# Optimization experiments

Hardware: AMD Instinct MI355X
Metric: run time of the kernel (lower is better)

Reference implementation:

```python
import jax, jax.numpy as jnp
import numpy as np

BS, S, DIM, H = 4, 2048, 1024, 16
DH = DIM // H  # 64


def setup_inputs() -> dict:
    key = jax.random.key(0)
    ks = jax.random.split(key, 12)
    def lin(k, fan_in):
        bound = 1.0 / np.sqrt(fan_in)
        kw, kb = jax.random.split(k)
        W = jax.random.uniform(kw, (DIM, DIM), jnp.float32, -bound, bound)
        b = jax.random.uniform(kb, (DIM,), jnp.float32, -bound, bound)
        return W, b
    Wq, bq = lin(ks[0], DIM)
    Wk, bk = lin(ks[1], DIM)
    Wv, bv = lin(ks[2], DIM)
    Wo, bo = lin(ks[3], DIM)
    return {
        "query": jax.random.normal(ks[4], (BS, S, DIM), jnp.float32),
        "key": jax.random.normal(ks[5], (BS, S, DIM), jnp.float32),
        "value": jax.random.normal(ks[6], (BS, S, DIM), jnp.float32),
        "mask": jnp.ones((BS, S), jnp.int32),
        "Wq": Wq, "bq": bq, "Wk": Wk, "bk": bk,
        "Wv": Wv, "bv": bv, "Wo": Wo, "bo": bo,
    }


def reference(query, key, value, mask, Wq, bq, Wk, bk, Wv, bv, Wo, bo):
    bs, q_len, dim = query.shape
    def shape_heads(x):  # (bs, s, dim) -> (bs, H, s, DH)
        return x.reshape(bs, -1, H, DH).transpose(0, 2, 1, 3)
    # Linear projections (torch Linear: x @ W.T + b)
    q = shape_heads(query @ Wq.T + bq)
    k = shape_heads(key @ Wk.T + bk)
    v = shape_heads(value @ Wv.T + bv)
    q = q / jnp.sqrt(jnp.asarray(DH, q.dtype))
    # scores: (bs, H, q_len, k_len)
    scores = jnp.einsum('bhqd,bhkd->bhqk', q, k)
    neg = jnp.asarray(-jnp.inf, scores.dtype)
    pad = (mask == 0)[:, None, None, :]  # (bs,1,1,k_len)
    scores = jnp.where(pad, neg, scores)
    weights = jax.nn.softmax(scores, axis=-1)
    # dropout is identity in eval mode (reference is deterministic)
    context = jnp.einsum('bhqk,bhkd->bhqd', weights, v)
    context = context.transpose(0, 2, 1, 3).reshape(bs, q_len, dim)
    return context @ Wo.T + bo
```

## Files before the change

kernel.cpp:

```cpp
#include <hip/hip_runtime.h>
#include <hip/hip_bf16.h>
#include <math.h>

#define BSZ 4
#define SEQ 2048
#define DIMN 1024
#define NHEAD 16
#define DHEAD 64
#define MROWS (BSZ*SEQ)

typedef __bf16 bf16x8 __attribute__((ext_vector_type(8)));
typedef float  f32x4  __attribute__((ext_vector_type(4)));
typedef float  f32x16 __attribute__((ext_vector_type(16)));
typedef float  fvec4  __attribute__((ext_vector_type(4)));
typedef short  s16x4  __attribute__((ext_vector_type(4)));
typedef short  s16x8  __attribute__((ext_vector_type(8)));

__device__ __forceinline__ short f2bf(float v) {
  __hip_bfloat16 b = __float2bfloat16(v);
  return *reinterpret_cast<short*>(&b);
}
__device__ __forceinline__ float bf2f(short s) {
  __hip_bfloat16 b = *reinterpret_cast<__hip_bfloat16*>(&s);
  return __bfloat162float(b);
}

__device__ __forceinline__ void gld_lds16(const void* g, void* l) {
  __builtin_amdgcn_global_load_lds((const __attribute__((address_space(1))) void*)g,
                                   (__attribute__((address_space(3))) void*)l, 16, 0, 0);
}

#define QSC 0.18033688011112042f

__global__ __launch_bounds__(256) void pack_w4(
    const float* __restrict__ Wq, const float* __restrict__ Wk,
    const float* __restrict__ Wv, const float* __restrict__ Wo,
    short* __restrict__ WQh, short* __restrict__ WKh,
    short* __restrict__ WVh, short* __restrict__ WOh, short* __restrict__ WOl,
    long n)
{
  long i = ((long)blockIdx.x * 256 + threadIdx.x) * 4;
  if (i >= n) return;
  int which = blockIdx.y;
  if (which == 3) {
    fvec4 v = *(const fvec4*)&Wo[i];
    s16x4 h, l;
#pragma unroll
    for (int j = 0; j < 4; ++j) {
      short hb = f2bf(v[j]);
      h[j] = hb;
      l[j] = f2bf(v[j] - bf2f(hb));
    }
    *(s16x4*)&WOh[i] = h;
    *(s16x4*)&WOl[i] = l;
  } else {
    const float* src = which == 0 ? Wq : (which == 1 ? Wk : Wv);
    short* dst = which == 0 ? WQh : (which == 1 ? WKh : WVh);
    float sc = which == 0 ? QSC : 1.f;
    fvec4 v = *(const fvec4*)&src[i];
    s16x4 h;
#pragma unroll
    for (int j = 0; j < 4; ++j) h[j] = f2bf(v[j] * sc);
    *(s16x4*)&dst[i] = h;
  }
}

__global__ __launch_bounds__(256) void pack_hi3(
    const float* __restrict__ q, const float* __restrict__ k,
    const float* __restrict__ v,
    short* __restrict__ xq, short* __restrict__ xk, short* __restrict__ xv,
    long n)
{
  long i = ((long)blockIdx.x * 256 + threadIdx.x) * 4;
  if (i >= n) return;
  const float* src = blockIdx.y == 0 ? q : (blockIdx.y == 1 ? k : v);
  short* dst = blockIdx.y == 0 ? xq : (blockIdx.y == 1 ? xk : xv);
  fvec4 x = *(const fvec4*)&src[i];
  s16x4 h;
#pragma unroll
  for (int j = 0; j < 4; ++j) h[j] = f2bf(x[j]);
  *(s16x4*)&dst[i] = h;
}

__global__ __launch_bounds__(256) void maskbias_k(
    const int* __restrict__ mask, float* __restrict__ mb, int n)
{
  int i = blockIdx.x * 256 + threadIdx.x;
  if (i < n) mb[i] = mask[i] ? 0.f : -1e30f;
}

__global__ __launch_bounds__(64) void mask_flags(
    const int* __restrict__ mask, int* __restrict__ flg)
{
  int c = blockIdx.x;
  int base = (c >> 4) * SEQ + (c & 15) * 128;
  int m0 = mask[base + threadIdx.x];
  int m1 = mask[base + 64 + threadIdx.x];
  unsigned long long bal = __ballot(m0 != 0 && m1 != 0);
  if (threadIdx.x == 0) flg[c] = (bal == ~0ull) ? 1 : 0;
}

__global__ __launch_bounds__(256) void gemm_h(
    const short* __restrict__ A, const short* __restrict__ B,
    const float* __restrict__ bias, float bscale,
    float* __restrict__ Cf, short* __restrict__ Cb,
    int M, int N, int K, int mode)
{
  __shared__ __align__(16) short sA[128*32];
  __shared__ __align__(16) short sB[128*32];
  const int t = threadIdx.x;
  const int ln = t & 15, quad = (t & 63) >> 4, w = t >> 6;
  const int wm = w >> 1, wn = w & 1;
  const int m0 = blockIdx.y * 128, n0 = blockIdx.x * 128;
  const int lrow = t >> 2;
  const int lko = (((t & 3) ^ ((t >> 3) & 3))) * 8;
  const int fsw = ((ln >> 1) & 3);
  f32x4 acc[4][4];
#pragma unroll
  for (int i = 0; i < 4; ++i)
#pragma unroll
    for (int j = 0; j < 4; ++j) acc[i][j] = (f32x4){0.f,0.f,0.f,0.f};

  for (int k0 = 0; k0 < K; k0 += 32) {
    __syncthreads();
#pragma unroll
    for (int u = 0; u < 2; ++u) {
      int row = u*64 + lrow;
      gld_lds16(A + (size_t)(m0+row)*K + k0 + lko, sA + u*2048 + t*8);
      gld_lds16(B + (size_t)(n0+row)*K + k0 + lko, sB + u*2048 + t*8);
    }
    __syncthreads();
    bf16x8 af[4], bfr[4];
#pragma unroll
    for (int mt = 0; mt < 4; ++mt)
      af[mt] = *(bf16x8*)&sA[(wm*64 + mt*16 + ln)*32 + (quad ^ fsw)*8];
#pragma unroll
    for (int nt = 0; nt < 4; ++nt)
      bfr[nt] = *(bf16x8*)&sB[(wn*64 + nt*16 + ln)*32 + (quad ^ fsw)*8];
#pragma unroll
    for (int mt = 0; mt < 4; ++mt)
#pragma unroll
      for (int nt = 0; nt < 4; ++nt)
        acc[mt][nt] = __builtin_amdgcn_mfma_f32_16x16x32_bf16(af[mt], bfr[nt], acc[mt][nt], 0, 0, 0);
  }
#pragma unroll
  for (int nt = 0; nt < 4; ++nt) {
    int col = n0 + wn*64 + nt*16 + ln;
    float bv = bias[col] * bscale;
    if (mode == 2) {
      int hd = col >> 6, dd = col & 63;
#pragma unroll
      for (int mt = 0; mt < 4; ++mt) {
        int sg = m0 + wm*64 + mt*16 + quad*4;
        int b = sg >> 11, s = sg & 2047;
        s16x4 h;
#pragma unroll
        for (int r = 0; r < 4; ++r) h[r] = f2bf(acc[mt][nt][r] + bv);
        *(s16x4*)&Cb[((size_t)((b*16 + hd)*64 + dd))*SEQ + s] = h;
      }
    } else {
#pragma unroll
      for (int mt = 0; mt < 4; ++mt)
#pragma unroll
        for (int r = 0; r < 4; ++r) {
          int row = m0 + wm*64 + mt*16 + quad*4 + r;
          float val = acc[mt][nt][r] + bv;
          if (mode == 0) Cf[(size_t)row*N + col] = val;
          else           Cb[(size_t)row*N + col] = f2bf(val);
        }
    }
  }
}

__global__ __launch_bounds__(256) void gemm_sp(
    const short* __restrict__ Ah, const short* __restrict__ Al,
    const short* __restrict__ Bh, const short* __restrict__ Bl,
    const float* __restrict__ bias, float bscale,
    float* __restrict__ C, int M, int N, int K)
{
  __shared__ __align__(16) short sA[2*128*32];
  __shared__ __align__(16) short sB[2*128*32];
  const int t = threadIdx.x;
  const int ln = t & 15, quad = (t & 63) >> 4, w = t >> 6;
  const int wm = w >> 1, wn = w & 1;
  const int m0 = blockIdx.y * 128, n0 = blockIdx.x * 128;
  const int lrow = t >> 2;
  const int lko = (((t & 3) ^ ((t >> 3) & 3))) * 8;
  const int fsw = ((ln >> 1) & 3);
  f32x4 acc[4][4];
#pragma unroll
  for (int i = 0; i < 4; ++i)
#pragma unroll
    for (int j = 0; j < 4; ++j) acc[i][j] = (f32x4){0.f,0.f,0.f,0.f};

  for (int k0 = 0; k0 < K; k0 += 32) {
    __syncthreads();
#pragma unroll
    for (int u = 0; u < 2; ++u) {
      int row = u*64 + lrow;
      gld_lds16(Ah + (size_t)(m0+row)*K + k0 + lko, sA + u*2048 + t*8);
      gld_lds16(Al + (size_t)(m0+row)*K + k0 + lko, sA + 4096 + u*2048 + t*8);
      gld_lds16(Bh + (size_t)(n0+row)*K + k0 + lko, sB + u*2048 + t*8);
      gld_lds16(Bl + (size_t)(n0+row)*K + k0 + lko, sB + 4096 + u*2048 + t*8);
    }
    __syncthreads();
    bf16x8 ah[4], al[4], bh[4], bl[4];
#pragma unroll
    for (int mt = 0; mt < 4; ++mt) {
      int r = wm*64 + mt*16 + ln;
      ah[mt] = *(bf16x8*)&sA[r*32 + (quad ^ fsw)*8];
      al[mt] = *(bf16x8*)&sA[4096 + r*32 + (quad ^ fsw)*8];
    }
#pragma unroll
    for (int nt = 0; nt < 4; ++nt) {
      int r = wn*64 + nt*16 + ln;
      bh[nt] = *(bf16x8*)&sB[r*32 + (quad ^ fsw)*8];
      bl[nt] = *(bf16x8*)&sB[4096 + r*32 + (quad ^ fsw)*8];
    }
#pragma unroll
    for (int mt = 0; mt < 4; ++mt)
#pragma unroll
      for (int nt = 0; nt < 4; ++nt) {
        acc[mt][nt] = __builtin_amdgcn_mfma_f32_16x16x32_bf16(ah[mt], bh[nt], acc[mt][nt], 0, 0, 0);
        acc[mt][nt] = __builtin_amdgcn_mfma_f32_16x16x32_bf16(ah[mt], bl[nt], acc[mt][nt], 0, 0, 0);
        acc[mt][nt] = __builtin_amdgcn_mfma_f32_16x16x32_bf16(al[mt], bh[nt], acc[mt][nt], 0, 0, 0);
      }
  }
#pragma unroll
  for (int nt = 0; nt < 4; ++nt) {
    float bv = bias[n0 + wn*64 + nt*16 + ln] * bscale;
#pragma unroll
    for (int mt = 0; mt < 4; ++mt)
#pragma unroll
      for (int r = 0; r < 4; ++r)
        C[(size_t)(m0 + wm*64 + mt*16 + quad*4 + r)*N + (n0 + wn*64 + nt*16 + ln)] =
            acc[mt][nt][r] + bv;
  }
}

__global__ __launch_bounds__(256, 3) void attn_32(
    const short* __restrict__ QB, const short* __restrict__ KB,
    const short* __restrict__ VT, const float* __restrict__ mb,
    const int* __restrict__ flg,
    short* __restrict__ CTXh, short* __restrict__ CTXl)
{
  __shared__ __align__(16) short lds[16384];
  short* sK = lds;
  short* sV = lds + 8192;

  const int t = threadIdx.x;
  const int l31 = t & 31, hi = (t >> 5) & 1, w = t >> 6;
  const int gb = blockIdx.x;
  const int chunk = gb >> 3, qt128 = chunk & 15, bh = ((chunk >> 4) << 3) + (gb & 7);
  const int b = bh >> 4, hd = bh & 15;

#pragma unroll
  for (int i = 0; i < 4; ++i) {
    int u = i*256 + t;
    int row = u >> 3, gr = (u & 7) ^ (row & 7);
    gld_lds16(QB + ((size_t)(b*SEQ + qt128*128 + row))*DIMN + hd*64 + gr*8,
              sK + u*8);
  }
  __syncthreads();
  const int q = w*32 + l31;
  bf16x8 qf[4];
#pragma unroll
  for (int ks = 0; ks < 4; ++ks)
    qf[ks] = *(bf16x8*)&sK[q*64 + ((ks*2 + hi) ^ (q & 7))*8];

  f32x16 o_acc[2] = {};
  float m_run = -1e30f, l_run = 0.f;

  for (int kt = 0; kt < SEQ/128; ++kt) {
    __syncthreads();
#pragma unroll
    for (int i = 0; i < 4; ++i) {
      int u = i*256 + t;
      { int row = u >> 3, gr = (u & 7) ^ (row & 7);
        gld_lds16(KB + ((size_t)(b*SEQ + kt*128 + row))*DIMN + hd*64 + gr*8,
                  sK + u*8); }
      { int d = u >> 4, gr = (u & 15) ^ (d & 15);
        gld_lds16(VT + ((size_t)(bh*64 + d))*SEQ + kt*128 + gr*8,
                  sV + u*8); }
    }
    __syncthreads();

    f32x16 sacc[4] = {};
#pragma unroll
    for (int ks = 0; ks < 4; ++ks)
#pragma unroll
      for (int mt = 0; mt < 4; ++mt) {
        int kc = mt*32 + l31;
        bf16x8 kf = *(bf16x8*)&sK[kc*64 + ((ks*2 + hi) ^ (kc & 7))*8];
        sacc[mt] = __builtin_amdgcn_mfma_f32_32x32x16_bf16(kf, qf[ks], sacc[mt], 0, 0, 0);
      }

    if (!flg[b*16 + kt]) {
#pragma unroll
      for (int mt = 0; mt < 4; ++mt)
#pragma unroll
        for (int r = 0; r < 16; ++r)
          sacc[mt][r] += mb[b*SEQ + kt*128 + mt*32 + (r&3) + 8*(r>>2) + 4*hi];
    }

    float tmax = -1e30f;
#pragma unroll
    for (int mt = 0; mt < 4; ++mt)
#pragma unroll
      for (int r = 0; r < 16; ++r) tmax = fmaxf(tmax, sacc[mt][r]);
    tmax = fmaxf(tmax, __shfl_xor(tmax, 32));

    if (!__all(tmax <= m_run + 8.f)) {
      float mnew = fmaxf(m_run, tmax);
      float alpha = exp2f(m_run - mnew);
      l_run *= alpha;
#pragma unroll
      for (int dt = 0; dt < 2; ++dt)
#pragma unroll
        for (int r = 0; r < 16; ++r) o_acc[dt][r] *= alpha;
      m_run = mnew;
    }

    float rs = 0.f;
#pragma unroll
    for (int mt = 0; mt < 4; ++mt)
#pragma unroll
      for (int r = 0; r < 16; ++r) {
        float p = exp2f(sacc[mt][r] - m_run);
        sacc[mt][r] = p;
        rs += p;
      }
    rs += __shfl_xor(rs, 32);
    l_run += rs;

#pragma unroll
    for (int mt = 0; mt < 4; ++mt) {
      unsigned wv[8];
#pragma unroll
      for (int i = 0; i < 8; ++i) {
        float plo = sacc[mt][2*i], phi = sacc[mt][2*i+1];
        asm("v_cvt_pk_bf16_f32 %0, %1, %2" : "=v"(wv[i]) : "v"(plo), "v"(phi));
      }
#pragma unroll
      for (int h = 0; h < 2; ++h) {
        unsigned f0 = wv[h*4+0], f1 = wv[h*4+1], f2 = wv[h*4+2], f3 = wv[h*4+3];
        asm volatile("v_permlane32_swap_b32 %0, %1" : "+v"(f0), "+v"(f2));
        asm volatile("v_permlane32_swap_b32 %0, %1" : "+v"(f1), "+v"(f3));
        union { unsigned u[4]; bf16x8 v; } pu;
        pu.u[0] = f0; pu.u[1] = f1; pu.u[2] = f2; pu.u[3] = f3;
        const int kcs = mt*2 + h;
#pragma unroll
        for (int dt = 0; dt < 2; ++dt) {
          int d = dt*32 + l31;
          bf16x8 vf = *(bf16x8*)&sV[d*128 + ((kcs*2 + hi) ^ (d & 15))*8];
          o_acc[dt] = __builtin_amdgcn_mfma_f32_32x32x16_bf16(vf, pu.v, o_acc[dt], 0, 0, 0);
        }
      }
    }
  }

  float invl = (l_run > 0.f) ? 1.f / l_run : 0.f;
  const size_t rowbase = (size_t)(b*SEQ + qt128*128 + q)*DIMN + hd*64;
#pragma unroll
  for (int dt = 0; dt < 2; ++dt)
#pragma unroll
    for (int rg = 0; rg < 4; ++rg) {
      s16x4 hq, lq;
#pragma unroll
      for (int r2 = 0; r2 < 4; ++r2) {
        float val = o_acc[dt][rg*4 + r2] * invl;
        short hb = f2bf(val);
        hq[r2] = hb;
        lq[r2] = f2bf(val - bf2f(hb));
      }
      size_t idx = rowbase + dt*32 + rg*8 + hi*4;
      *(s16x4*)&CTXh[idx] = hq;
      *(s16x4*)&CTXl[idx] = lq;
    }
}

__global__ __launch_bounds__(256) void gemm_bt(
    const float* __restrict__ X, const float* __restrict__ W,
    const float* __restrict__ bias, float* __restrict__ C,
    int M, int N, int K)
{
  __shared__ __align__(16) float Xs[16][68];
  __shared__ __align__(16) float Ws[16][68];
  const int t  = threadIdx.x;
  const int tx = t & 15, ty = t >> 4;
  const int m0 = blockIdx.y << 6, n0 = blockIdx.x << 6;
  const int ldr = t >> 2;
  const int lk  = (t & 3) << 2;
  float acc[4][4] = {{0.f}};
  const float* Xp = X + (size_t)(m0 + ldr) * K + lk;
  const float* Wp = W + (size_t)(n0 + ldr) * K + lk;
  for (int k0 = 0; k0 < K; k0 += 16) {
    float4 xa = *(const float4*)(Xp + k0);
    float4 wa = *(const float4*)(Wp + k0);
    Xs[lk+0][ldr]=xa.x; Xs[lk+1][ldr]=xa.y; Xs[lk+2][ldr]=xa.z; Xs[lk+3][ldr]=xa.w;
    Ws[lk+0][ldr]=wa.x; Ws[lk+1][ldr]=wa.y; Ws[lk+2][ldr]=wa.z; Ws[lk+3][ldr]=wa.w;
    __syncthreads();
#pragma unroll
    for (int kk = 0; kk < 16; ++kk) {
      float4 a4 = *(const float4*)&Xs[kk][ty<<2];
      float4 b4 = *(const float4*)&Ws[kk][tx<<2];
      float av[4] = {a4.x, a4.y, a4.z, a4.w};
      float bv[4] = {b4.x, b4.y, b4.z, b4.w};
#pragma unroll
      for (int i = 0; i < 4; ++i)
#pragma unroll
        for (int j = 0; j < 4; ++j)
          acc[i][j] = fmaf(av[i], bv[j], acc[i][j]);
    }
    __syncthreads();
  }
  float4 bb4 = *(const float4*)&bias[n0 + (tx<<2)];
  const float bv[4] = {bb4.x, bb4.y, bb4.z, bb4.w};
#pragma unroll
  for (int i = 0; i < 4; ++i) {
    float4 o;
    o.x = acc[i][0]+bv[0]; o.y = acc[i][1]+bv[1];
    o.z = acc[i][2]+bv[2]; o.w = acc[i][3]+bv[3];
    *(float4*)&C[(size_t)(m0 + (ty<<2) + i) * N + n0 + (tx<<2)] = o;
  }
}

__global__ __launch_bounds__(256) void attn_fwd(
    const float* __restrict__ Q, const float* __restrict__ Kbuf,
    const float* __restrict__ Vbuf, const int* __restrict__ mask,
    float* __restrict__ CTX)
{
  __shared__ __align__(16) float Qs[64][68];
  __shared__ __align__(16) float KPs[64][68];
  __shared__ __align__(16) float Vs[64][68];
  const int t  = threadIdx.x;
  const int tx = t & 15, ty = t >> 4;
  const int qt = blockIdx.x;
  const int bh = blockIdx.y;
  const int b  = bh >> 4, h = bh & 15;
  const int ldr = t >> 2;
  const int lcb = (t & 3) << 2;
  const float* Qp = Q + (size_t)(b*SEQ + (qt<<6)) * DIMN + h*DHEAD;
#pragma unroll
  for (int u = 0; u < 4; ++u) {
    int kb = lcb + (u<<4);
    float4 q4 = *(const float4*)(Qp + (size_t)ldr*DIMN + kb);
    Qs[kb+0][ldr]=q4.x; Qs[kb+1][ldr]=q4.y; Qs[kb+2][ldr]=q4.z; Qs[kb+3][ldr]=q4.w;
  }
  float mrow[4], lsum[4], o[4][4];
#pragma unroll
  for (int i = 0; i < 4; ++i) {
    mrow[i] = -1e30f; lsum[i] = 0.f;
#pragma unroll
    for (int j = 0; j < 4; ++j) o[i][j] = 0.f;
  }
  const int qrow0 = ty << 2;
  const int col0  = tx << 2;
  for (int kt = 0; kt < SEQ/64; ++kt) {
    __syncthreads();
    const float* Kp = Kbuf + (size_t)(b*SEQ + (kt<<6)) * DIMN + h*DHEAD;
    const float* Vp = Vbuf + (size_t)(b*SEQ + (kt<<6)) * DIMN + h*DHEAD;
#pragma unroll
    for (int u = 0; u < 4; ++u) {
      int kb = lcb + (u<<4);
      float4 k4 = *(const float4*)(Kp + (size_t)ldr*DIMN + kb);
      KPs[kb+0][ldr]=k4.x; KPs[kb+1][ldr]=k4.y; KPs[kb+2][ldr]=k4.z; KPs[kb+3][ldr]=k4.w;
      float4 v4 = *(const float4*)(Vp + (size_t)ldr*DIMN + kb);
      *(float4*)&Vs[ldr][kb] = v4;
    }
    __syncthreads();
    float s[4][4] = {{0.f}};
#pragma unroll 8
    for (int kk = 0; kk < 64; ++kk) {
      float4 a4 = *(const float4*)&Qs[kk][qrow0];
      float4 b4 = *(const float4*)&KPs[kk][col0];
      float av[4] = {a4.x, a4.y, a4.z, a4.w};
      float bv[4] = {b4.x, b4.y, b4.z, b4.w};
#pragma unroll
      for (int i = 0; i < 4; ++i)
#pragma unroll
        for (int j = 0; j < 4; ++j)
          s[i][j] = fmaf(av[i], bv[j], s[i][j]);
    }
    int mk[4];
#pragma unroll
    for (int j = 0; j < 4; ++j) mk[j] = mask[b*SEQ + (kt<<6) + col0 + j];
    float p[4][4];
#pragma unroll
    for (int i = 0; i < 4; ++i) {
#pragma unroll
      for (int j = 0; j < 4; ++j)
        s[i][j] = mk[j] ? s[i][j]*0.125f : -1e30f;
      float tm = fmaxf(fmaxf(s[i][0], s[i][1]), fmaxf(s[i][2], s[i][3]));
#pragma unroll
      for (int off = 8; off >= 1; off >>= 1)
        tm = fmaxf(tm, __shfl_xor(tm, off, 64));
      float mnew  = fmaxf(mrow[i], tm);
      float aa = __expf(mrow[i] - mnew);
      mrow[i] = mnew;
      float rsum = 0.f;
#pragma unroll
      for (int j = 0; j < 4; ++j) {
        float pv = __expf(s[i][j] - mnew);
        p[i][j] = pv; rsum += pv;
      }
#pragma unroll
      for (int off = 8; off >= 1; off >>= 1)
        rsum += __shfl_xor(rsum, off, 64);
      lsum[i] = lsum[i]*aa + rsum;
#pragma unroll
      for (int j = 0; j < 4; ++j) o[i][j] *= aa;
    }
    __syncthreads();
#pragma unroll
    for (int i = 0; i < 4; ++i)
#pragma unroll
      for (int j = 0; j < 4; ++j)
        KPs[col0 + j][qrow0 + i] = p[i][j];
    __syncthreads();
#pragma unroll 8
    for (int kk = 0; kk < 64; ++kk) {
      float4 a4 = *(const float4*)&KPs[kk][qrow0];
      float4 v4 = *(const float4*)&Vs[kk][col0];
      float av[4] = {a4.x, a4.y, a4.z, a4.w};
      float vv[4] = {v4.x, v4.y, v4.z, v4.w};
#pragma unroll
      for (int i = 0; i < 4; ++i)
#pragma unroll
        for (int j = 0; j < 4; ++j)
          o[i][j] = fmaf(av[i], vv[j], o[i][j]);
    }
  }
  float* Cp = CTX + (size_t)(b*SEQ + (qt<<6)) * DIMN + h*DHEAD;
#pragma unroll
  for (int i = 0; i < 4; ++i) {
    float inv = lsum[i] > 0.f ? 1.0f/lsum[i] : 0.f;
    float4 ov;
    ov.x = o[i][0]*inv; ov.y = o[i][1]*inv;
    ov.z = o[i][2]*inv; ov.w = o[i][3]*inv;
    *(float4*)(Cp + (size_t)(qrow0 + i)*DIMN + col0) = ov;
  }
}

extern "C" void kernel_launch(void* const* d_in, const int* in_sizes, int n_in,
                              void* d_out, int out_size, void* d_ws, size_t ws_size,
                              hipStream_t stream)
{
  const float* query = (const float*)d_in[0];
  const float* key   = (const float*)d_in[1];
  const float* value = (const float*)d_in[2];
  const int*   mask  = (const int*)d_in[3];
  const float* Wq = (const float*)d_in[4];
  const float* bq = (const float*)d_in[5];
  const float* Wk = (const float*)d_in[6];
  const float* bk = (const float*)d_in[7];
  const float* Wv = (const float*)d_in[8];
  const float* bv = (const float*)d_in[9];
  const float* Wo = (const float*)d_in[10];
  const float* bo = (const float*)d_in[11];
  float* out = (float*)d_out;

  const size_t E  = (size_t)MROWS * DIMN;
  const size_t WE = (size_t)DIMN * DIMN;

  const size_t o_XB   = 5*WE*2;
  const size_t o_QB   = o_XB   + 3*E*2;
  const size_t o_KB   = o_QB   + E*2;
  const size_t o_VT   = o_KB   + E*2;
  const size_t o_CTXh = o_VT   + E*2;
  const size_t o_CTXl = o_CTXh + E*2;
  const size_t o_MB   = o_CTXl + E*2;
  const size_t o_FLG  = o_MB   + MROWS*4;
  const size_t NEED   = o_FLG  + 64*4;

  if (ws_size < NEED) {
    const size_t n = E;
    float* Qb = (float*)d_ws;
    float* Kb = Qb + n;
    float* Vb = Kb + n;
    float* Cb = Vb + n;
    dim3 gg(DIMN/64, MROWS/64), blk(256);
    hipLaunchKernelGGL(gemm_bt, gg, blk, 0, stream, query, Wq, bq, Qb, MROWS, DIMN, DIMN);
    hipLaunchKernelGGL(gemm_bt, gg, blk, 0, stream, key,   Wk, bk, Kb, MROWS, DIMN, DIMN);
    hipLaunchKernelGGL(gemm_bt, gg, blk, 0, stream, value, Wv, bv, Vb, MROWS, DIMN, DIMN);
    dim3 ga(SEQ/64, BSZ*NHEAD);
    hipLaunchKernelGGL(attn_fwd, ga, blk, 0, stream, Qb, Kb, Vb, mask, Cb);
    hipLaunchKernelGGL(gemm_bt, gg, blk, 0, stream, Cb, Wo, bo, out, MROWS, DIMN, DIMN);
    return;
  }

  char* Wp = (char*)d_ws;
  short* WQh = (short*)Wp;
  short* WKh = WQh + WE;
  short* WVh = WQh + 2*WE;
  short* WOh = WQh + 3*WE;
  short* WOl = WQh + 4*WE;
  short* XBq  = (short*)(Wp + o_XB);
  short* XBk  = XBq + E;
  short* XBv  = XBk + E;
  short* QB   = (short*)(Wp + o_QB);
  short* KB   = (short*)(Wp + o_KB);
  short* VT   = (short*)(Wp + o_VT);
  short* CTXh = (short*)(Wp + o_CTXh);
  short* CTXl = (short*)(Wp + o_CTXl);
  float* MB   = (float*)(Wp + o_MB);
  int*   FLG  = (int*)(Wp + o_FLG);

  dim3 blk(256);
  dim3 gW(WE/1024, 4), gX(E/1024, 3);
  dim3 gg(DIMN/128, MROWS/128);
  dim3 gat(BSZ*NHEAD*SEQ/128);

  hipLaunchKernelGGL(pack_w4, gW, blk, 0, stream, Wq, Wk, Wv, Wo,
                     WQh, WKh, WVh, WOh, WOl, (long)WE);
  hipLaunchKernelGGL(maskbias_k, dim3(MROWS/256), blk, 0, stream, mask, MB, MROWS);
  hipLaunchKernelGGL(mask_flags, dim3(64), dim3(64), 0, stream, mask, FLG);
  hipLaunchKernelGGL(pack_hi3, gX, blk, 0, stream, query, key, value,
                     XBq, XBk, XBv, (long)E);

  hipLaunchKernelGGL(gemm_h, gg, blk, 0, stream, XBq, WQh, bq, QSC,
                     (float*)nullptr, QB, MROWS, DIMN, DIMN, 1);
  hipLaunchKernelGGL(gemm_h, gg, blk, 0, stream, XBk, WKh, bk, 1.f,
                     (float*)nullptr, KB, MROWS, DIMN, DIMN, 1);
  hipLaunchKernelGGL(gemm_h, gg, blk, 0, stream, XBv, WVh, bv, 1.f,
                     (float*)nullptr, VT, MROWS, DIMN, DIMN, 2);

  hipLaunchKernelGGL(attn_32, gat, blk, 0, stream, QB, KB, VT, MB, FLG, CTXh, CTXl);

  hipLaunchKernelGGL(gemm_sp, gg, blk, 0, stream, CTXh, CTXl, WOh, WOl, bo, 1.f,
                     out, MROWS, DIMN, DIMN);
}
```

Measured before the change: 433.5 us.

## Double-buffer K/V tiles in attention kernel to overlap loads with MFMA

The attention kernel now keeps two LDS buffers for K and V and prefetches the next key tile while computing on the current one, with a single barrier per iteration instead of two. Q is staged in a separate LDS region, and s_setprio raises wave priority around the MFMA sections. The row max is computed with a tree reduction instead of a serial chain. The LDS footprint doubles to 64KB and occupancy hint drops from 3 to 2 blocks per CU, which trades latency hiding across waves for overlap within a block.

```diff
diff --git a/kernel.cpp b/kernel.cpp
--- a/kernel.cpp
+++ b/kernel.cpp
@@ -28,6 +28,17 @@
 __device__ __forceinline__ void gld_lds16(const void* g, void* l) {
   __builtin_amdgcn_global_load_lds((const __attribute__((address_space(1))) void*)g,
                                    (__attribute__((address_space(3))) void*)l, 16, 0, 0);
+}
+
+__device__ __forceinline__ float max16(const f32x16 v) {
+  float m0 = fmaxf(fmaxf(v[0], v[1]),  v[2]);
+  float m1 = fmaxf(fmaxf(v[3], v[4]),  v[5]);
+  float m2 = fmaxf(fmaxf(v[6], v[7]),  v[8]);
+  float m3 = fmaxf(fmaxf(v[9], v[10]), v[11]);
+  float m4 = fmaxf(fmaxf(v[12], v[13]), v[14]);
+  float m5 = fmaxf(v[15], m0);
+  float m6 = fmaxf(fmaxf(m1, m2), m3);
+  return fmaxf(fmaxf(m4, m5), m6);
 }
 
 #define QSC 0.18033688011112042f
@@ -238,15 +249,13 @@
   }
 }
 
-__global__ __launch_bounds__(256, 3) void attn_32(
+__global__ __launch_bounds__(256, 2) void attn_db(
     const short* __restrict__ QB, const short* __restrict__ KB,
     const short* __restrict__ VT, const float* __restrict__ mb,
     const int* __restrict__ flg,
     short* __restrict__ CTXh, short* __restrict__ CTXl)
 {
-  __shared__ __align__(16) short lds[16384];
-  short* sK = lds;
-  short* sV = lds + 8192;
+  __shared__ __align__(16) short lds[32768];
 
   const int t = threadIdx.x;
   const int l31 = t & 31, hi = (t >> 5) & 1, w = t >> 6;
@@ -259,41 +268,60 @@
     int u = i*256 + t;
     int row = u >> 3, gr = (u & 7) ^ (row & 7);
     gld_lds16(QB + ((size_t)(b*SEQ + qt128*128 + row))*DIMN + hd*64 + gr*8,
-              sK + u*8);
+              lds + 16384 + u*8);
+  }
+#pragma unroll
+  for (int i = 0; i < 4; ++i) {
+    int u = i*256 + t;
+    { int row = u >> 3, gr = (u & 7) ^ (row & 7);
+      gld_lds16(KB + ((size_t)(b*SEQ + row))*DIMN + hd*64 + gr*8,
+                lds + u*8); }
+    { int d = u >> 4, gr = (u & 15) ^ (d & 15);
+      gld_lds16(VT + ((size_t)(bh*64 + d))*SEQ + gr*8,
+                lds + 8192 + u*8); }
   }
   __syncthreads();
   const int q = w*32 + l31;
   bf16x8 qf[4];
 #pragma unroll
   for (int ks = 0; ks < 4; ++ks)
-    qf[ks] = *(bf16x8*)&sK[q*64 + ((ks*2 + hi) ^ (q & 7))*8];
+    qf[ks] = *(const bf16x8*)&lds[16384 + q*64 + ((ks*2 + hi) ^ (q & 7))*8];
+  asm volatile("s_waitcnt lgkmcnt(0)" ::: "memory");
+  __builtin_amdgcn_s_barrier();
 
   f32x16 o_acc[2] = {};
   float m_run = -1e30f, l_run = 0.f;
+  int cur = 0;
 
   for (int kt = 0; kt < SEQ/128; ++kt) {
-    __syncthreads();
-#pragma unroll
-    for (int i = 0; i < 4; ++i) {
-      int u = i*256 + t;
-      { int row = u >> 3, gr = (u & 7) ^ (row & 7);
-        gld_lds16(KB + ((size_t)(b*SEQ + kt*128 + row))*DIMN + hd*64 + gr*8,
-                  sK + u*8); }
-      { int d = u >> 4, gr = (u & 15) ^ (d & 15);
-        gld_lds16(VT + ((size_t)(bh*64 + d))*SEQ + kt*128 + gr*8,
-                  sV + u*8); }
-    }
-    __syncthreads();
+    if (kt + 1 < SEQ/128) {
+      short* dK = lds + (cur ^ 1)*16384;
+      short* dV = dK + 8192;
+#pragma unroll
+      for (int i = 0; i < 4; ++i) {
+        int u = i*256 + t;
+        { int row = u >> 3, gr = (u & 7) ^ (row & 7);
+          gld_lds16(KB + ((size_t)(b*SEQ + (kt+1)*128 + row))*DIMN + hd*64 + gr*8,
+                    dK + u*8); }
+        { int d = u >> 4, gr = (u & 15) ^ (d & 15);
+          gld_lds16(VT + ((size_t)(bh*64 + d))*SEQ + (kt+1)*128 + gr*8,
+                    dV + u*8); }
+      }
+    }
+    const short* sK = lds + cur*16384;
+    const short* sV = sK + 8192;
 
     f32x16 sacc[4] = {};
+    __builtin_amdgcn_s_setprio(1);
 #pragma unroll
     for (int ks = 0; ks < 4; ++ks)
 #pragma unroll
       for (int mt = 0; mt < 4; ++mt) {
         int kc = mt*32 + l31;
-        bf16x8 kf = *(bf16x8*)&sK[kc*64 + ((ks*2 + hi) ^ (kc & 7))*8];
+        bf16x8 kf = *(const bf16x8*)&sK[kc*64 + ((ks*2 + hi) ^ (kc & 7))*8];
         sacc[mt] = __builtin_amdgcn_mfma_f32_32x32x16_bf16(kf, qf[ks], sacc[mt], 0, 0, 0);
       }
+    __builtin_amdgcn_s_setprio(0);
 
     if (!flg[b*16 + kt]) {
 #pragma unroll
@@ -303,11 +331,8 @@
           sacc[mt][r] += mb[b*SEQ + kt*128 + mt*32 + (r&3) + 8*(r>>2) + 4*hi];
     }
 
-    float tmax = -1e30f;
-#pragma unroll
-    for (int mt = 0; mt < 4; ++mt)
-#pragma unroll
-      for (int r = 0; r < 16; ++r) tmax = fmaxf(tmax, sacc[mt][r]);
+    float tmax = fmaxf(fmaxf(max16(sacc[0]), max16(sacc[1])),
+                       fmaxf(max16(sacc[2]), max16(sacc[3])));
     tmax = fmaxf(tmax, __shfl_xor(tmax, 32));
 
     if (!__all(tmax <= m_run + 8.f)) {
@@ -333,6 +358,7 @@
     rs += __shfl_xor(rs, 32);
     l_run += rs;
 
+    __builtin_amdgcn_s_setprio(1);
 #pragma unroll
     for (int mt = 0; mt < 4; ++mt) {
       unsigned wv[8];
@@ -352,11 +378,16 @@
 #pragma unroll
         for (int dt = 0; dt < 2; ++dt) {
           int d = dt*32 + l31;
-          bf16x8 vf = *(bf16x8*)&sV[d*128 + ((kcs*2 + hi) ^ (d & 15))*8];
+          bf16x8 vf = *(const bf16x8*)&sV[d*128 + ((kcs*2 + hi) ^ (d & 15))*8];
           o_acc[dt] = __builtin_amdgcn_mfma_f32_32x32x16_bf16(vf, pu.v, o_acc[dt], 0, 0, 0);
         }
       }
     }
+    __builtin_amdgcn_s_setprio(0);
+
+    asm volatile("s_waitcnt vmcnt(0)" ::: "memory");
+    __builtin_amdgcn_s_barrier();
+    cur ^= 1;
   }
 
   float invl = (l_run > 0.f) ? 1.f / l_run : 0.f;
@@ -625,7 +656,7 @@
   hipLaunchKernelGGL(gemm_h, gg, blk, 0, stream, XBv, WVh, bv, 1.f,
                      (float*)nullptr, VT, MROWS, DIMN, DIMN, 2);
 
-  hipLaunchKernelGGL(attn_32, gat, blk, 0, stream, QB, KB, VT, MB, FLG, CTXh, CTXl);
+  hipLaunchKernelGGL(attn_db, gat, blk, 0, stream, QB, KB, VT, MB, FLG, CTXh, CTXl);
 
   hipLaunchKernelGGL(gemm_sp, gg, blk, 0, stream, CTXh, CTXl, WOh, WOl, bo, 1.f,
                      out, MROWS, DIMN, DIMN);
```

New measurement: 441.8 us. About the same (+1.9%).

## Split attention key tile into halves with max folded into MFMA init and setprio

Applied to the files above, without the earlier changes.

The attention inner loop now handles each 128-key tile as two 64-key halves. Score accumulators start at -m_run, so the running-max subtraction rides on the MFMA accumulate, and the online-softmax update runs per half. s_setprio is raised around the MFMA sections and the max reduction is rebalanced into a tree. The goal is lower register pressure from the halved score buffer and shorter dependency chains in the softmax, at the cost of more frequent rescale checks and extra shuffles per tile.

```diff
diff --git a/kernel.cpp b/kernel.cpp
--- a/kernel.cpp
+++ b/kernel.cpp
@@ -28,6 +28,17 @@
 __device__ __forceinline__ void gld_lds16(const void* g, void* l) {
   __builtin_amdgcn_global_load_lds((const __attribute__((address_space(1))) void*)g,
                                    (__attribute__((address_space(3))) void*)l, 16, 0, 0);
+}
+
+__device__ __forceinline__ float max16(const f32x16 v) {
+  float m0 = fmaxf(fmaxf(v[0], v[1]),  v[2]);
+  float m1 = fmaxf(fmaxf(v[3], v[4]),  v[5]);
+  float m2 = fmaxf(fmaxf(v[6], v[7]),  v[8]);
+  float m3 = fmaxf(fmaxf(v[9], v[10]), v[11]);
+  float m4 = fmaxf(fmaxf(v[12], v[13]), v[14]);
+  float m5 = fmaxf(v[15], m0);
+  float m6 = fmaxf(fmaxf(m1, m2), m3);
+  return fmaxf(fmaxf(m4, m5), m6);
 }
 
 #define QSC 0.18033688011112042f
@@ -238,7 +249,7 @@
   }
 }
 
-__global__ __launch_bounds__(256, 3) void attn_32(
+__global__ __launch_bounds__(256, 3) void attn_hp(
     const short* __restrict__ QB, const short* __restrict__ KB,
     const short* __restrict__ VT, const float* __restrict__ mb,
     const int* __restrict__ flg,
@@ -266,10 +277,10 @@
   bf16x8 qf[4];
 #pragma unroll
   for (int ks = 0; ks < 4; ++ks)
-    qf[ks] = *(bf16x8*)&sK[q*64 + ((ks*2 + hi) ^ (q & 7))*8];
+    qf[ks] = *(const bf16x8*)&sK[q*64 + ((ks*2 + hi) ^ (q & 7))*8];
 
   f32x16 o_acc[2] = {};
-  float m_run = -1e30f, l_run = 0.f;
+  float m_run = 0.f, l_run = 0.f;
 
   for (int kt = 0; kt < SEQ/128; ++kt) {
     __syncthreads();
@@ -285,77 +296,103 @@
     }
     __syncthreads();
 
-    f32x16 sacc[4] = {};
-#pragma unroll
-    for (int ks = 0; ks < 4; ++ks)
-#pragma unroll
-      for (int mt = 0; mt < 4; ++mt) {
-        int kc = mt*32 + l31;
-        bf16x8 kf = *(bf16x8*)&sK[kc*64 + ((ks*2 + hi) ^ (kc & 7))*8];
-        sacc[mt] = __builtin_amdgcn_mfma_f32_32x32x16_bf16(kf, qf[ks], sacc[mt], 0, 0, 0);
-      }
-
-    if (!flg[b*16 + kt]) {
-#pragma unroll
-      for (int mt = 0; mt < 4; ++mt)
-#pragma unroll
-        for (int r = 0; r < 16; ++r)
-          sacc[mt][r] += mb[b*SEQ + kt*128 + mt*32 + (r&3) + 8*(r>>2) + 4*hi];
-    }
-
-    float tmax = -1e30f;
-#pragma unroll
-    for (int mt = 0; mt < 4; ++mt)
-#pragma unroll
-      for (int r = 0; r < 16; ++r) tmax = fmaxf(tmax, sacc[mt][r]);
-    tmax = fmaxf(tmax, __shfl_xor(tmax, 32));
-
-    if (!__all(tmax <= m_run + 8.f)) {
-      float mnew = fmaxf(m_run, tmax);
-      float alpha = exp2f(m_run - mnew);
-      l_run *= alpha;
-#pragma unroll
-      for (int dt = 0; dt < 2; ++dt)
-#pragma unroll
-        for (int r = 0; r < 16; ++r) o_acc[dt][r] *= alpha;
-      m_run = mnew;
-    }
-
-    float rs = 0.f;
-#pragma unroll
-    for (int mt = 0; mt < 4; ++mt)
-#pragma unroll
-      for (int r = 0; r < 16; ++r) {
-        float p = exp2f(sacc[mt][r] - m_run);
-        sacc[mt][r] = p;
-        rs += p;
-      }
-    rs += __shfl_xor(rs, 32);
-    l_run += rs;
-
-#pragma unroll
-    for (int mt = 0; mt < 4; ++mt) {
-      unsigned wv[8];
-#pragma unroll
-      for (int i = 0; i < 8; ++i) {
-        float plo = sacc[mt][2*i], phi = sacc[mt][2*i+1];
-        asm("v_cvt_pk_bf16_f32 %0, %1, %2" : "=v"(wv[i]) : "v"(plo), "v"(phi));
-      }
-#pragma unroll
-      for (int h = 0; h < 2; ++h) {
-        unsigned f0 = wv[h*4+0], f1 = wv[h*4+1], f2 = wv[h*4+2], f3 = wv[h*4+3];
-        asm volatile("v_permlane32_swap_b32 %0, %1" : "+v"(f0), "+v"(f2));
-        asm volatile("v_permlane32_swap_b32 %0, %1" : "+v"(f1), "+v"(f3));
-        union { unsigned u[4]; bf16x8 v; } pu;
-        pu.u[0] = f0; pu.u[1] = f1; pu.u[2] = f2; pu.u[3] = f3;
-        const int kcs = mt*2 + h;
-#pragma unroll
-        for (int dt = 0; dt < 2; ++dt) {
-          int d = dt*32 + l31;
-          bf16x8 vf = *(bf16x8*)&sV[d*128 + ((kcs*2 + hi) ^ (d & 15))*8];
-          o_acc[dt] = __builtin_amdgcn_mfma_f32_32x32x16_bf16(vf, pu.v, o_acc[dt], 0, 0, 0);
+    const bool allv = flg[b*16 + kt] != 0;
+
+#pragma unroll
+    for (int hf = 0; hf < 2; ++hf) {
+      f32x16 s2[2];
+      {
+        float mneg = -m_run;
+#pragma unroll
+        for (int mt2 = 0; mt2 < 2; ++mt2)
+#pragma unroll
+          for (int r = 0; r < 16; ++r) s2[mt2][r] = mneg;
+      }
+
+      __builtin_amdgcn_s_setprio(1);
+#pragma unroll
+      for (int ks = 0; ks < 4; ++ks)
+#pragma unroll
+        for (int mt2 = 0; mt2 < 2; ++mt2) {
+          int kc = (hf*2 + mt2)*32 + l31;
+          bf16x8 kf = *(const bf16x8*)&sK[kc*64 + ((ks*2 + hi) ^ (kc & 7))*8];
+          s2[mt2] = __builtin_amdgcn_mfma_f32_32x32x16_bf16(kf, qf[ks], s2[mt2], 0, 0, 0);
         }
-      }
+      __builtin_amdgcn_s_setprio(0);
+
+      if (!allv) {
+#pragma unroll
+        for (int mt2 = 0; mt2 < 2; ++mt2)
+#pragma unroll
+          for (int r = 0; r < 16; ++r)
+            s2[mt2][r] += mb[b*SEQ + kt*128 + (hf*2 + mt2)*32 + (r&3) + 8*(r>>2) + 4*hi];
+      }
+
+      float tb = fmaxf(max16(s2[0]), max16(s2[1]));
+      tb = fmaxf(tb, __shfl_xor(tb, 32));
+
+      float rs0 = 0.f, rs1 = 0.f;
+      if (__builtin_expect(!__all(tb <= 8.f), 0)) {
+        float delta = fmaxf(tb, 0.f);
+        float al = exp2f(-delta);
+        l_run *= al;
+#pragma unroll
+        for (int dt = 0; dt < 2; ++dt)
+#pragma unroll
+          for (int r = 0; r < 16; ++r) o_acc[dt][r] *= al;
+        m_run += delta;
+#pragma unroll
+        for (int mt2 = 0; mt2 < 2; ++mt2)
+#pragma unroll
+          for (int r = 0; r < 16; ++r) {
+            float p = exp2f(s2[mt2][r] - delta);
+            s2[mt2][r] = p;
+            if (r & 1) rs1 += p; else rs0 += p;
+          }
+      } else {
+#pragma unroll
+        for (int mt2 = 0; mt2 < 2; ++mt2)
+#pragma unroll
+          for (int r = 0; r < 16; ++r) {
+            float p = exp2f(s2[mt2][r]);
+            s2[mt2][r] = p;
+            if (r & 1) rs1 += p; else rs0 += p;
+          }
+      }
+      float rs = rs0 + rs1;
+      rs += __shfl_xor(rs, 32);
+      l_run += rs;
+
+      __builtin_amdgcn_s_setprio(1);
+#pragma unroll
+      for (int mt2 = 0; mt2 < 2; ++mt2) {
+#pragma unroll
+        for (int h = 0; h < 2; ++h) {
+          unsigned w0, w1, w2, w3;
+          {
+            float a0 = s2[mt2][h*8+0], a1 = s2[mt2][h*8+1];
+            float a2 = s2[mt2][h*8+2], a3 = s2[mt2][h*8+3];
+            float a4 = s2[mt2][h*8+4], a5 = s2[mt2][h*8+5];
+            float a6 = s2[mt2][h*8+6], a7 = s2[mt2][h*8+7];
+            asm("v_cvt_pk_bf16_f32 %0, %1, %2" : "=v"(w0) : "v"(a0), "v"(a1));
+            asm("v_cvt_pk_bf16_f32 %0, %1, %2" : "=v"(w1) : "v"(a2), "v"(a3));
+            asm("v_cvt_pk_bf16_f32 %0, %1, %2" : "=v"(w2) : "v"(a4), "v"(a5));
+            asm("v_cvt_pk_bf16_f32 %0, %1, %2" : "=v"(w3) : "v"(a6), "v"(a7));
+          }
+          asm("v_permlane32_swap_b32 %0, %1" : "+v"(w0), "+v"(w2));
+          asm("v_permlane32_swap_b32 %0, %1" : "+v"(w1), "+v"(w3));
+          union { unsigned u[4]; bf16x8 v; } pu;
+          pu.u[0] = w0; pu.u[1] = w1; pu.u[2] = w2; pu.u[3] = w3;
+          const int kcs = (hf*2 + mt2)*2 + h;
+#pragma unroll
+          for (int dt = 0; dt < 2; ++dt) {
+            int d = dt*32 + l31;
+            bf16x8 vf = *(const bf16x8*)&sV[d*128 + ((kcs*2 + hi) ^ (d & 15))*8];
+            o_acc[dt] = __builtin_amdgcn_mfma_f32_32x32x16_bf16(vf, pu.v, o_acc[dt], 0, 0, 0);
+          }
+        }
+      }
+      __builtin_amdgcn_s_setprio(0);
     }
   }
 
@@ -625,7 +662,7 @@
   hipLaunchKernelGGL(gemm_h, gg, blk, 0, stream, XBv, WVh, bv, 1.f,
                      (float*)nullptr, VT, MROWS, DIMN, DIMN, 2);
 
-  hipLaunchKernelGGL(attn_32, gat, blk, 0, stream, QB, KB, VT, MB, FLG, CTXh, CTXl);
+  hipLaunchKernelGGL(attn_hp, gat, blk, 0, stream, QB, KB, VT, MB, FLG, CTXh, CTXl);
 
   hipLaunchKernelGGL(gemm_sp, gg, blk, 0, stream, CTXh, CTXl, WOh, WOl, bo, 1.f,
                      out, MROWS, DIMN, DIMN);
```

After: 572.3 us. 32.0% more time.
